# Kernel optimization log

Measured on AMD Instinct MI355X. Metric: run time of the kernel, lower is better.

## Reference

```python
import jax, jax.numpy as jnp
import numpy as np

STRIDE = 1
PADDING = 1
GROUPS = 1


def quantize_ternary(w):
    # scale = detached mean |w|, clamped; STE: identity gradient through rounding
    scale = jnp.maximum(jax.lax.stop_gradient(jnp.abs(w).mean()), 1e-5)
    w_scaled = w / scale
    w_tern = jax.lax.stop_gradient(jnp.clip(jnp.round(w_scaled), -1.0, 1.0) - w_scaled) + w_scaled
    return w_tern * scale


def setup_inputs() -> dict:
    key = jax.random.key(0)
    k1, k2, k3 = jax.random.split(key, 3)
    x = jax.random.normal(k1, (16, 256, 128, 128), dtype=jnp.float32)
    weight = jax.random.normal(k2, (256, 256, 3, 3), dtype=jnp.float32) * 0.05
    bias = jax.random.normal(k3, (256,), dtype=jnp.float32) * 0.05
    return {"x": x, "weight": weight, "bias": bias}


def reference(x, weight, bias):
    w_q = quantize_ternary(weight)
    out = jax.lax.conv_general_dilated(
        x, w_q,
        window_strides=(STRIDE, STRIDE),
        padding=[(PADDING, PADDING), (PADDING, PADDING)],
        dimension_numbers=("NCHW", "OIHW", "NCHW"),
        feature_group_count=GROUPS,
    )
    return out + bias[None, :, None, None]
```

## Files before the change

kernel.cpp:

```cpp
#include <hip/hip_runtime.h>

#define N_ 16
#define C_ 256
#define H_ 128
#define W_ 128
#define O_ 256
#define HW_ (H_ * W_)
#define CHW_ (C_ * HW_)
#define WELEMS (O_ * C_ * 9)
#define SX (6.2f / 127.0f)

#define XH 130
#define XW 130
#define XB_BYTES ((long)N_ * XH * 4 * XW * 64)
#define XB_OFF (2l << 20)
#define WS_NEED (XB_OFF + XB_BYTES)

#define ROWB 4224
#define BUFB (6 * ROWB)
#define ABUF 8192

typedef short bf16x8 __attribute__((ext_vector_type(8)));
typedef int i32x4 __attribute__((ext_vector_type(4)));
typedef float f32x4 __attribute__((ext_vector_type(4)));

#define GLOAD_LDS16(g, l)                                                     \
  __builtin_amdgcn_global_load_lds(                                           \
      (const __attribute__((address_space(1))) unsigned int*)(g),             \
      (__attribute__((address_space(3))) unsigned int*)(l), 16, 0, 0)

__global__ void absum_k(const float* __restrict__ w, float* __restrict__ sum) {
  int tid = blockIdx.x * blockDim.x + threadIdx.x;
  float s = 0.f;
  for (int i = tid; i < WELEMS; i += gridDim.x * blockDim.x) s += fabsf(w[i]);
  #pragma unroll
  for (int off = 32; off > 0; off >>= 1) s += __shfl_down(s, off, 64);
  if ((threadIdx.x & 63) == 0) atomicAdd(sum, s);
}

__global__ void aux_k(const float* __restrict__ x,
                      const float* __restrict__ w,
                      const float* __restrict__ sum,
                      signed char* __restrict__ wqA,
                      unsigned char* __restrict__ xbb) {
  const int b = blockIdx.x;
  const int t = threadIdx.x;

  if (b < 4096) {
    const int wh = b & 1, h = (b >> 1) & 127, n = b >> 8;
    const int wl = t & 63, cg = t >> 6;
    const int wcol = (wh << 6) + wl;
    const float* s0 = x + ((long)n * C_ + cg * 64) * HW_ + h * W_ + wcol;
    const int mw = ((wcol + 1) >> 1) & 3;
    unsigned char* lp =
        xbb + ((((long)n * XH + (h + 1)) * 4 + cg) * XW + (wcol + 1)) * 64;
    #pragma unroll
    for (int sub = 0; sub < 4; ++sub) {
      signed char pk[16];
      #pragma unroll
      for (int e = 0; e < 16; ++e) {
        float v = __builtin_nontemporal_load(&s0[(long)(sub * 16 + e) * HW_]);
        float q = rintf(v * (1.0f / SX));
        q = fminf(127.f, fmaxf(-127.f, q));
        pk[e] = (signed char)(int)q;
      }
      *(i32x4*)(lp + ((sub ^ mw) << 4)) = __builtin_bit_cast(i32x4, *(i32x4*)pk);
    }
  } else if (b < 6400) {
    const int i = (b - 4096) * 256 + t;
    if (i >= WELEMS) return;
    float scale = fmaxf(sum[0] * (1.0f / (float)WELEMS), 1e-5f);
    int kk = i % 9;
    int c = (i / 9) % C_;
    int o = i / (9 * C_);
    float q = rintf(w[i] / scale);
    q = fminf(1.f, fmaxf(-1.f, q));
    const int ohalf = o >> 7, ob = o & 127;
    const int cch = c >> 6, j = (c >> 4) & 3, e = c & 15;
    const long unit = (((long)(ohalf * 4 + cch) * 9 + kk) * 512) + ob * 4 + j;
    wqA[unit * 16 + e] = (signed char)q;
  } else {
    const int i = (b - 6400) * 256 + t;
    if (i >= 33280) return;
    long line;
    if (i < 16640) {
      int wq = i % 130; int tt = i / 130;
      int cg = tt & 3; tt >>= 2;
      int hh = tt & 1; int nn = tt >> 1;
      line = (((long)nn * XH + hh * 129) * 4 + cg) * XW + wq;
    } else {
      int jj = i - 16640;
      int side = jj & 1; int tt = jj >> 1;
      int cg = tt & 3; tt >>= 2;
      int hp = tt % 130; int nn = tt / 130;
      line = (((long)nn * XH + hp) * 4 + cg) * XW + side * 129;
    }
    f32x4 z = (f32x4){0.f, 0.f, 0.f, 0.f};
    #pragma unroll
    for (int j4 = 0; j4 < 4; ++j4)
      *(f32x4*)(xbb + line * 64 + j4 * 16) = z;
  }
}

__global__ void quant_fb_k(const float* __restrict__ w, const float* __restrict__ sum,
                           unsigned short* __restrict__ wp) {
  int i = blockIdx.x * blockDim.x + threadIdx.x;
  if (i >= WELEMS) return;
  float scale = fmaxf(sum[0] * (1.0f / (float)WELEMS), 1e-5f);
  int kk = i % 9;
  int c = (i / 9) % C_;
  int o = i / (9 * C_);
  float q = rintf(w[i] / scale);
  q = fminf(1.f, fmaxf(-1.f, q));
  wp[(kk * O_ + o) * C_ + c] = __builtin_bit_cast(unsigned short, (__bf16)q);
}

__global__ void __launch_bounds__(512, 4)
conv_k(const unsigned char* __restrict__ xbb,
       const float* __restrict__ bias,
       const signed char* __restrict__ wqA,
       const float* __restrict__ sum,
       float* __restrict__ out) {
  __shared__ __attribute__((aligned(128))) unsigned char Lds[2 * BUFB + 2 * ABUF];
  unsigned char* Xsl = Lds;
  unsigned char* Asl = Lds + 2 * BUFB;

  const int xcd = blockIdx.x & 7, jb = blockIdx.x >> 3;
  const int sub = jb & 3;
  const int ohalf = sub >> 1, wblk = sub & 1;
  const int pid = (xcd << 6) + (jb >> 2);
  const int n = pid >> 5;
  const int h0 = (pid & 31) << 2;
  const int w0 = wblk << 6;
  const int o_blk = ohalf << 7;

  const int tid = threadIdx.x;
  const int wid = tid >> 6, lane = tid & 63;
  const int l15 = lane & 15, g = lane >> 4;
  const int wmd = (wid >> 2);
  const int r = wid & 3;

  const int ob = tid >> 2, aj = tid & 3;
  const int awoff = ob * 64 + ((aj ^ ((ob >> 1) & 3)) << 4);
  const uint4* wA = (const uint4*)wqA + (long)ohalf * (4 * 9 * 512) + tid;

  const int abase = (wmd * 64 + l15) * 64 + ((g ^ ((l15 >> 1) & 3)) << 4);

  i32x4 acc[4][4];
  #pragma unroll
  for (int i = 0; i < 4; ++i)
    #pragma unroll
    for (int jj = 0; jj < 4; ++jj) acc[i][jj] = (i32x4){0, 0, 0, 0};

  auto stageX = [&](int b, int cg) {
    if (wid < 6) {
      const unsigned char* src =
          xbb + ((((long)n * XH + h0 + wid) * 4 + cg) * XW + w0) * 64;
      unsigned char* dst = Xsl + b * BUFB + wid * ROWB;
      #pragma unroll
      for (int it = 0; it < 4; ++it)
        GLOAD_LDS16(src + (it * 64 + lane) * 16, dst + it * 1024);
      if (lane < 8)
        GLOAD_LDS16(src + (256 + lane) * 16, dst + 4096);
    }
  };

  uint4 arA, arB;

  stageX(0, 0);
  __builtin_amdgcn_sched_barrier(0);
  arA = wA[0];
  arB = wA[512];
  __builtin_amdgcn_sched_barrier(0);

#define TAP(T, DT, S)                                                          \
  {                                                                            \
    if ((S) == 0) {                                                            \
      __builtin_amdgcn_sched_barrier(0);                                       \
      asm volatile("s_waitcnt vmcnt(2)" ::: "memory");                         \
      __builtin_amdgcn_sched_barrier(0);                                       \
    }                                                                          \
    unsigned char* Ab = Asl + (((DT) + (S)) & 1) * ABUF;                       \
    *(uint4*)(Ab + awoff) = (((DT) + (S)) & 1) ? arB : arA;                    \
    {                                            \
      int ns = (S) + 2, nt = (T);                                              \
      if (ns >= 9) { ns -= 9; nt += 1; }                                       \
      if (nt < 4) {                                                            \
        uint4 nv = wA[(nt * 9 + ns) << 9];                                     \
        if (((DT) + (S)) & 1) arB = nv; else arA = nv;                         \
      }                                                                        \
    }                                                                          \
    if ((S) == 6) {                                                            \
      if ((T) < 3) {                                                           \
        __builtin_amdgcn_sched_barrier(0);                                     \
        stageX(1 - (DT), (T) + 1);                                             \
        __builtin_amdgcn_sched_barrier(0);                                     \
      }                                                                        \
    }                                                                          \
    asm volatile("s_waitcnt lgkmcnt(0)" ::: "memory");                         \
    __builtin_amdgcn_sched_barrier(0);                                         \
    __builtin_amdgcn_s_barrier();                                              \
    __builtin_amdgcn_sched_barrier(0);                                         \
    {                       \
      const int ky = (S) / 3, kx = (S)-ky * 3;                                 \
      const unsigned char* Xb = Xsl + (DT)*BUFB + (r + ky) * ROWB;             \
      i32x4 a0 = *(const i32x4*)(Ab + abase);                                  \
      i32x4 a1 = *(const i32x4*)(Ab + abase + 1024);                           \
      i32x4 a2 = *(const i32x4*)(Ab + abase + 2048);                           \
      i32x4 a3 = *(const i32x4*)(Ab + abase + 3072);                           \
      i32x4 bb[4];                                                             \
      _Pragma("unroll")                                                        \
      for (int ni = 0; ni < 4; ++ni) {                                         \
        const int wq = (ni << 4) + l15 + kx;                                   \
        const int sl = g ^ ((wq >> 1) & 3);                                    \
        bb[ni] = *(const i32x4*)(Xb + wq * 64 + sl * 16);                      \
      }                                                                        \
      __builtin_amdgcn_s_setprio(1);                                           \
      _Pragma("unroll")                                                        \
      for (int ni = 0; ni < 4; ++ni) {                                         \
        acc[0][ni] = __builtin_amdgcn_mfma_i32_16x16x64_i8(a0, bb[ni], acc[0][ni], 0, 0, 0); \
        acc[1][ni] = __builtin_amdgcn_mfma_i32_16x16x64_i8(a1, bb[ni], acc[1][ni], 0, 0, 0); \
        acc[2][ni] = __builtin_amdgcn_mfma_i32_16x16x64_i8(a2, bb[ni], acc[2][ni], 0, 0, 0); \
        acc[3][ni] = __builtin_amdgcn_mfma_i32_16x16x64_i8(a3, bb[ni], acc[3][ni], 0, 0, 0); \
      }                                                                        \
      __builtin_amdgcn_s_setprio(0);                                           \
    }                                                                          \
  }

#define CHUNK(T, DT)                                                           \
  TAP(T, DT, 0) TAP(T, DT, 1) TAP(T, DT, 2) TAP(T, DT, 3) TAP(T, DT, 4)        \
  TAP(T, DT, 5) TAP(T, DT, 6) TAP(T, DT, 7) TAP(T, DT, 8)

  for (int tt = 0; tt < 2; ++tt) {
    const int te = tt * 2;
    CHUNK(te, 0)
    const int to = te + 1;
    CHUNK(to, 1)
  }
#undef CHUNK
#undef TAP

  const float scale = fmaxf(sum[0] * (1.0f / (float)WELEMS), 1e-5f) * SX;
  const int h_out = h0 + r;
  #pragma unroll
  for (int mi = 0; mi < 4; ++mi) {
    #pragma unroll
    for (int q = 0; q < 4; ++q) {
      const int o = o_blk + wmd * 64 + (mi << 4) + (g << 2) + q;
      const float bv = bias[o];
      float* orow = out + ((long)n * O_ + o) * (long)HW_ + h_out * W_;
      #pragma unroll
      for (int ni = 0; ni < 4; ++ni) {
        const int wc = w0 + (ni << 4) + l15;
        orow[wc] = (float)acc[mi][ni][q] * scale + bv;
      }
    }
  }
}

#define LSTRIDE 80
#define LINES_FB 130
__global__ void __launch_bounds__(512, 4)
conv_fb(const float* __restrict__ x,
        const float* __restrict__ bias,
        const unsigned short* __restrict__ wp,
        const float* __restrict__ sum,
        float* __restrict__ out) {
  __shared__ __attribute__((aligned(128))) unsigned char Xs[4 * 130 * LSTRIDE];
  const int bid = blockIdx.x;
  const int pid = bid >> 1, ohalf = bid & 1;
  const int spid = (pid & 7) * 128 + (pid >> 3);
  const int n = spid >> 6;
  const int h0 = (spid & 63) << 1;
  const int o_blk = ohalf << 7;
  const int tid = threadIdx.x;
  if (tid < 128) {
    const int li = tid >> 5, sel = (tid >> 4) & 1, word = tid & 15;
    const int wq = sel ? 129 : 0;
    *(int*)(Xs + (li * LINES_FB + wq) * LSTRIDE + word * 4) = 0;
  }
  const int wid = tid >> 6, lane = tid & 63;
  const int l15 = lane & 15, g = lane >> 4;
  const int wmo = (wid >> 2) << 6;
  const int wsid = wid & 3, r = wsid >> 1, wbase = (wsid & 1) << 6;
  const int sw = tid & 127, sli = tid >> 7;
  const int h_in = h0 - 1 + sli;
  const bool inb = (unsigned)h_in < (unsigned)H_;
  const float* xsrc = x + (long)n * CHW_ + (long)h_in * W_ + sw;
  unsigned char* sdst = Xs + (sli * LINES_FB + sw + 1) * LSTRIDE;
  f32x4 acc[4][4];
  #pragma unroll
  for (int i = 0; i < 4; ++i)
    #pragma unroll
    for (int jj = 0; jj < 4; ++jj) acc[i][jj] = (f32x4){0.f, 0.f, 0.f, 0.f};
  for (int c0 = 0; c0 < C_; c0 += 32) {
    #pragma unroll
    for (int cg = 0; cg < 4; ++cg) {
      bf16x8 pk = (bf16x8){0, 0, 0, 0, 0, 0, 0, 0};
      if (inb) {
        const float* s = xsrc + (long)(c0 + (cg << 3)) * HW_;
        #pragma unroll
        for (int k = 0; k < 8; ++k)
          pk[k] = (short)__builtin_bit_cast(unsigned short, (__bf16)s[(long)k * HW_]);
      }
      *(bf16x8*)(sdst + (cg << 4)) = pk;
    }
    __syncthreads();
    #pragma unroll
    for (int kk = 0; kk < 9; ++kk) {
      const int ky = kk / 3, kx = kk - ky * 3;
      const int li = r + ky;
      const unsigned short* abase2 =
          wp + ((kk * O_ + o_blk + wmo + l15) * C_) + c0 + (g << 3);
      bf16x8 a[4];
      #pragma unroll
      for (int mi = 0; mi < 4; ++mi)
        a[mi] = *(const bf16x8*)(abase2 + (mi << 4) * C_);
      #pragma unroll
      for (int ni = 0; ni < 4; ++ni) {
        const int wq = wbase + (ni << 4) + l15 + kx;
        const bf16x8 bb = *(const bf16x8*)(&Xs[(li * LINES_FB + wq) * LSTRIDE + (g << 4)]);
        #pragma unroll
        for (int mi = 0; mi < 4; ++mi)
          acc[mi][ni] = __builtin_amdgcn_mfma_f32_16x16x32_bf16(a[mi], bb, acc[mi][ni], 0, 0, 0);
      }
    }
    __syncthreads();
  }
  const float scale = fmaxf(sum[0] * (1.0f / (float)WELEMS), 1e-5f);
  const int h_out = h0 + r;
  #pragma unroll
  for (int mi = 0; mi < 4; ++mi) {
    #pragma unroll
    for (int q = 0; q < 4; ++q) {
      const int o = o_blk + wmo + (mi << 4) + (g << 2) + q;
      const float bv = bias[o];
      float* orow = out + ((long)n * O_ + o) * (long)HW_ + h_out * W_;
      #pragma unroll
      for (int ni = 0; ni < 4; ++ni) {
        const int wc = wbase + (ni << 4) + l15;
        orow[wc] = acc[mi][ni][q] * scale + bv;
      }
    }
  }
}

extern "C" void kernel_launch(void* const* d_in, const int* in_sizes, int n_in,
                              void* d_out, int out_size, void* d_ws, size_t ws_size,
                              hipStream_t stream) {
  const float* x = (const float*)d_in[0];
  const float* w = (const float*)d_in[1];
  const float* bias = (const float*)d_in[2];
  float* out = (float*)d_out;
  float* sum = (float*)d_ws;

  hipMemsetAsync(d_ws, 0, 4, stream);
  absum_k<<<256, 256, 0, stream>>>(w, sum);

  if (ws_size >= (size_t)WS_NEED) {
    signed char* wqA = (signed char*)((char*)d_ws + 64);
    unsigned char* xbb = (unsigned char*)d_ws + XB_OFF;
    aux_k<<<6530, 256, 0, stream>>>(x, w, sum, wqA, xbb);
    conv_k<<<2048, 512, 0, stream>>>(xbb, bias, wqA, sum, out);
  } else {
    unsigned short* wp = (unsigned short*)((char*)d_ws + 64);
    quant_fb_k<<<WELEMS / 256, 256, 0, stream>>>(w, sum, wp);
    conv_fb<<<2048, 512, 0, stream>>>(x, bias, wp, sum, out);
  }
}
```

Measured before the change: 248.2 us.

## Load weight fragments directly from global memory instead of staging through LDS

The ternary int8 weights are now laid out in MFMA fragment order, so each lane reads its A operands straight from global memory (and L2) rather than going through a double-buffered LDS stage. This drops the per-tap LDS store, the s_barrier and the lgkmcnt wait, leaving one barrier per channel chunk, and frees the LDS the weight buffers used. The cost is global-load latency on every tap with no explicit prefetch, plus redundant weight reads across waves and blocks. Setprio hints and the fine-grained vmcnt pipelining are also removed.

```diff
diff --git a/kernel.cpp b/kernel.cpp
--- a/kernel.cpp
+++ b/kernel.cpp
@@ -18,7 +18,6 @@
 
 #define ROWB 4224
 #define BUFB (6 * ROWB)
-#define ABUF 8192
 
 typedef short bf16x8 __attribute__((ext_vector_type(8)));
 typedef int i32x4 __attribute__((ext_vector_type(4)));
@@ -41,7 +40,7 @@
 __global__ void aux_k(const float* __restrict__ x,
                       const float* __restrict__ w,
                       const float* __restrict__ sum,
-                      signed char* __restrict__ wqA,
+                      signed char* __restrict__ wq2,
                       unsigned char* __restrict__ xbb) {
   const int b = blockIdx.x;
   const int t = threadIdx.x;
@@ -75,10 +74,11 @@
     int o = i / (9 * C_);
     float q = rintf(w[i] / scale);
     q = fminf(1.f, fmaxf(-1.f, q));
-    const int ohalf = o >> 7, ob = o & 127;
-    const int cch = c >> 6, j = (c >> 4) & 3, e = c & 15;
-    const long unit = (((long)(ohalf * 4 + cch) * 9 + kk) * 512) + ob * 4 + j;
-    wqA[unit * 16 + e] = (signed char)q;
+    const int ohalf = o >> 7, wmdq = (o >> 6) & 1, mi = (o >> 4) & 3, l15q = o & 15;
+    const int chunk = c >> 6, g = (c >> 4) & 3, e = c & 15;
+    const long addr = ((((long)(ohalf * 2 + wmdq) * 4 + chunk) * 9 + kk) * 4 + mi) * 1024
+                      + l15q * 64 + g * 16 + e;
+    wq2[addr] = (signed char)q;
   } else {
     const int i = (b - 6400) * 256 + t;
     if (i >= 33280) return;
@@ -118,12 +118,10 @@
 __global__ void __launch_bounds__(512, 4)
 conv_k(const unsigned char* __restrict__ xbb,
        const float* __restrict__ bias,
-       const signed char* __restrict__ wqA,
+       const signed char* __restrict__ wq2,
        const float* __restrict__ sum,
        float* __restrict__ out) {
-  __shared__ __attribute__((aligned(128))) unsigned char Lds[2 * BUFB + 2 * ABUF];
-  unsigned char* Xsl = Lds;
-  unsigned char* Asl = Lds + 2 * BUFB;
+  __shared__ __attribute__((aligned(128))) unsigned char Xsl[2 * BUFB];
 
   const int xcd = blockIdx.x & 7, jb = blockIdx.x >> 3;
   const int sub = jb & 3;
@@ -140,11 +138,8 @@
   const int wmd = (wid >> 2);
   const int r = wid & 3;
 
-  const int ob = tid >> 2, aj = tid & 3;
-  const int awoff = ob * 64 + ((aj ^ ((ob >> 1) & 3)) << 4);
-  const uint4* wA = (const uint4*)wqA + (long)ohalf * (4 * 9 * 512) + tid;
-
-  const int abase = (wmd * 64 + l15) * 64 + ((g ^ ((l15 >> 1) & 3)) << 4);
+  const unsigned char* wA =
+      (const unsigned char*)wq2 + (long)(ohalf * 2 + wmd) * 147456 + l15 * 64 + g * 16;
 
   i32x4 acc[4][4];
   #pragma unroll
@@ -165,80 +160,44 @@
     }
   };
 
-  uint4 arA, arB;
-
   stageX(0, 0);
-  __builtin_amdgcn_sched_barrier(0);
-  arA = wA[0];
-  arB = wA[512];
-  __builtin_amdgcn_sched_barrier(0);
-
-#define TAP(T, DT, S)                                                          \
-  {                                                                            \
-    if ((S) == 0) {                                                            \
-      __builtin_amdgcn_sched_barrier(0);                                       \
-      asm volatile("s_waitcnt vmcnt(2)" ::: "memory");                         \
-      __builtin_amdgcn_sched_barrier(0);                                       \
-    }                                                                          \
-    unsigned char* Ab = Asl + (((DT) + (S)) & 1) * ABUF;                       \
-    *(uint4*)(Ab + awoff) = (((DT) + (S)) & 1) ? arB : arA;                    \
-    {                                            \
-      int ns = (S) + 2, nt = (T);                                              \
-      if (ns >= 9) { ns -= 9; nt += 1; }                                       \
-      if (nt < 4) {                                                            \
-        uint4 nv = wA[(nt * 9 + ns) << 9];                                     \
-        if (((DT) + (S)) & 1) arB = nv; else arA = nv;                         \
-      }                                                                        \
-    }                                                                          \
-    if ((S) == 6) {                                                            \
-      if ((T) < 3) {                                                           \
-        __builtin_amdgcn_sched_barrier(0);                                     \
-        stageX(1 - (DT), (T) + 1);                                             \
-        __builtin_amdgcn_sched_barrier(0);                                     \
-      }                                                                        \
-    }                                                                          \
-    asm volatile("s_waitcnt lgkmcnt(0)" ::: "memory");                         \
-    __builtin_amdgcn_sched_barrier(0);                                         \
-    __builtin_amdgcn_s_barrier();                                              \
-    __builtin_amdgcn_sched_barrier(0);                                         \
-    {                       \
-      const int ky = (S) / 3, kx = (S)-ky * 3;                                 \
-      const unsigned char* Xb = Xsl + (DT)*BUFB + (r + ky) * ROWB;             \
-      i32x4 a0 = *(const i32x4*)(Ab + abase);                                  \
-      i32x4 a1 = *(const i32x4*)(Ab + abase + 1024);                           \
-      i32x4 a2 = *(const i32x4*)(Ab + abase + 2048);                           \
-      i32x4 a3 = *(const i32x4*)(Ab + abase + 3072);                           \
-      i32x4 bb[4];                                                             \
-      _Pragma("unroll")                                                        \
-      for (int ni = 0; ni < 4; ++ni) {                                         \
-        const int wq = (ni << 4) + l15 + kx;                                   \
-        const int sl = g ^ ((wq >> 1) & 3);                                    \
-        bb[ni] = *(const i32x4*)(Xb + wq * 64 + sl * 16);                      \
-      }                                                                        \
-      __builtin_amdgcn_s_setprio(1);                                           \
-      _Pragma("unroll")                                                        \
-      for (int ni = 0; ni < 4; ++ni) {                                         \
-        acc[0][ni] = __builtin_amdgcn_mfma_i32_16x16x64_i8(a0, bb[ni], acc[0][ni], 0, 0, 0); \
-        acc[1][ni] = __builtin_amdgcn_mfma_i32_16x16x64_i8(a1, bb[ni], acc[1][ni], 0, 0, 0); \
-        acc[2][ni] = __builtin_amdgcn_mfma_i32_16x16x64_i8(a2, bb[ni], acc[2][ni], 0, 0, 0); \
-        acc[3][ni] = __builtin_amdgcn_mfma_i32_16x16x64_i8(a3, bb[ni], acc[3][ni], 0, 0, 0); \
-      }                                                                        \
-      __builtin_amdgcn_s_setprio(0);                                           \
-    }                                                                          \
-  }
-
-#define CHUNK(T, DT)                                                           \
-  TAP(T, DT, 0) TAP(T, DT, 1) TAP(T, DT, 2) TAP(T, DT, 3) TAP(T, DT, 4)        \
-  TAP(T, DT, 5) TAP(T, DT, 6) TAP(T, DT, 7) TAP(T, DT, 8)
-
-  for (int tt = 0; tt < 2; ++tt) {
-    const int te = tt * 2;
-    CHUNK(te, 0)
-    const int to = te + 1;
-    CHUNK(to, 1)
-  }
-#undef CHUNK
-#undef TAP
+  asm volatile("s_waitcnt vmcnt(0)" ::: "memory");
+  __builtin_amdgcn_s_barrier();
+
+  #pragma unroll
+  for (int t = 0; t < 4; ++t) {
+    if (t < 3) stageX((t + 1) & 1, t + 1);
+    const unsigned char* Xc = Xsl + (t & 1) * BUFB;
+    const unsigned char* wC = wA + (long)t * 36864;
+    #pragma unroll
+    for (int S = 0; S < 9; ++S) {
+      const int ky = S / 3, kx = S - ky * 3;
+      const unsigned char* wT = wC + S * 4096;
+      i32x4 a0 = *(const i32x4*)(wT);
+      i32x4 a1 = *(const i32x4*)(wT + 1024);
+      i32x4 a2 = *(const i32x4*)(wT + 2048);
+      i32x4 a3 = *(const i32x4*)(wT + 3072);
+      const unsigned char* Xb = Xc + (r + ky) * ROWB;
+      i32x4 bb[4];
+      #pragma unroll
+      for (int ni = 0; ni < 4; ++ni) {
+        const int wq = (ni << 4) + l15 + kx;
+        const int sl = g ^ ((wq >> 1) & 3);
+        bb[ni] = *(const i32x4*)(Xb + wq * 64 + sl * 16);
+      }
+      #pragma unroll
+      for (int ni = 0; ni < 4; ++ni) {
+        acc[0][ni] = __builtin_amdgcn_mfma_i32_16x16x64_i8(a0, bb[ni], acc[0][ni], 0, 0, 0);
+        acc[1][ni] = __builtin_amdgcn_mfma_i32_16x16x64_i8(a1, bb[ni], acc[1][ni], 0, 0, 0);
+        acc[2][ni] = __builtin_amdgcn_mfma_i32_16x16x64_i8(a2, bb[ni], acc[2][ni], 0, 0, 0);
+        acc[3][ni] = __builtin_amdgcn_mfma_i32_16x16x64_i8(a3, bb[ni], acc[3][ni], 0, 0, 0);
+      }
+    }
+    if (t < 3) {
+      asm volatile("s_waitcnt vmcnt(0)" ::: "memory");
+      __builtin_amdgcn_s_barrier();
+    }
+  }
 
   const float scale = fmaxf(sum[0] * (1.0f / (float)WELEMS), 1e-5f) * SX;
   const int h_out = h0 + r;
@@ -358,10 +317,10 @@
   absum_k<<<256, 256, 0, stream>>>(w, sum);
 
   if (ws_size >= (size_t)WS_NEED) {
-    signed char* wqA = (signed char*)((char*)d_ws + 64);
+    signed char* wq2 = (signed char*)((char*)d_ws + 64);
     unsigned char* xbb = (unsigned char*)d_ws + XB_OFF;
-    aux_k<<<6530, 256, 0, stream>>>(x, w, sum, wqA, xbb);
-    conv_k<<<2048, 512, 0, stream>>>(xbb, bias, wqA, sum, out);
+    aux_k<<<6530, 256, 0, stream>>>(x, w, sum, wq2, xbb);
+    conv_k<<<2048, 512, 0, stream>>>(xbb, bias, wq2, sum, out);
   } else {
     unsigned short* wp = (unsigned short*)((char*)d_ws + 64);
     quant_fb_k<<<WELEMS / 256, 256, 0, stream>>>(w, sum, wp);
```

Measured after the change: 325.7 us. +31.2%, slower.
